# Performance work log

Hardware: AMD Instinct MI355X
Metric: run time of the kernel (lower is better)

The kernel has to match this reference:

```python
import jax, jax.numpy as jnp
import numpy as np

B, N, F_IN, H, E = 8, 10000, 128, 128, 160000


def setup_inputs() -> dict:
    key = jax.random.key(0)
    ks = jax.random.split(key, 6)
    x = jax.random.normal(ks[0], (B, N, F_IN), dtype=jnp.float32)
    edge_index = jax.random.randint(ks[1], (2, E), 0, N, dtype=jnp.int64)
    # GCNConv params (glorot-ish scale), LayerNorm affine params
    W1 = jax.random.normal(ks[2], (F_IN, H), dtype=jnp.float32) / np.sqrt(F_IN)
    b1 = jnp.zeros((H,), dtype=jnp.float32)
    W2 = jax.random.normal(ks[3], (H, H), dtype=jnp.float32) / np.sqrt(H)
    b2 = jnp.zeros((H,), dtype=jnp.float32)
    ln_w = jnp.ones((H,), dtype=jnp.float32)
    ln_b = jnp.zeros((H,), dtype=jnp.float32)
    return {"x": x, "edge_index": edge_index, "W1": W1, "b1": b1,
            "W2": W2, "b2": b2, "ln_w": ln_w, "ln_b": ln_b}


def reference(x, edge_index, W1, b1, W2, b2, ln_w, ln_b):
    # x: [B, N, F]; edge_index: [2, E] shared across batch (tiled per graph
    # in the original via node offsets -> equivalent to vmapping over batch).
    n = x.shape[1]
    loops = jnp.arange(n, dtype=edge_index.dtype)
    src = jnp.concatenate([edge_index[0], loops])  # add self-loops (GCNConv default)
    dst = jnp.concatenate([edge_index[1], loops])
    # symmetric degree normalization: deg over targets with self-loops
    deg = jax.ops.segment_sum(jnp.ones(dst.shape[0], dtype=x.dtype), dst, num_segments=n)
    dinv = jnp.where(deg > 0, jax.lax.rsqrt(deg), 0.0)
    w_e = dinv[src] * dinv[dst]  # [E+N] per-edge norm

    def gcn_agg(h):  # h: [B, N, H] -> gather, scale, scatter-add
        msg = h[:, src, :] * w_e[None, :, None]  # [B, E+N, H]
        return jax.vmap(lambda m: jax.ops.segment_sum(m, dst, num_segments=n))(msg)

    h1 = jax.nn.relu(gcn_agg(x @ W1) + b1)
    h2 = gcn_agg(h1 @ W2) + b2
    # LayerNorm over last dim (eps=1e-5, torch default)
    mu = jnp.mean(h2, axis=-1, keepdims=True)
    var = jnp.mean(jnp.square(h2 - mu), axis=-1, keepdims=True)
    out = (h2 - mu) * jax.lax.rsqrt(var + 1e-5) * ln_w + ln_b
    return out  # [B, N, H]
```

## Files before the change

kernel.cpp:

```cpp
#include <hip/hip_runtime.h>
#include <hip/hip_bf16.h>

#define NNODES 10000
#define NB 8
#define NF 128
#define NE 160000

typedef __attribute__((ext_vector_type(8))) short  short8;
typedef __attribute__((ext_vector_type(8))) unsigned short ushort8;
typedef __attribute__((ext_vector_type(4))) float  f32x4;

__device__ __forceinline__ unsigned short f2b(float f) {
    union { float f; unsigned u; } v; v.f = f;
    unsigned r = v.u + 0x7FFF + ((v.u >> 16) & 1);
    return (unsigned short)(r >> 16);
}
__device__ __forceinline__ unsigned int f2b2(float a, float b) {
    union { __hip_bfloat162 h; unsigned int u; } v;
    v.h = __float22bfloat162_rn(make_float2(a, b));
    return v.u;
}
__device__ __forceinline__ float b2f_lo(unsigned u) {
    union { unsigned u; float f; } v; v.u = u << 16; return v.f;
}
__device__ __forceinline__ float b2f_hi(unsigned u) {
    union { unsigned u; float f; } v; v.u = u & 0xffff0000u; return v.f;
}


__global__ void k_zero(int* __restrict__ cnt, int* __restrict__ fill) {
    int i = blockIdx.x * blockDim.x + threadIdx.x;
    if (i < NNODES) cnt[i] = 0;
    else if (i < 2 * NNODES) fill[i - NNODES] = 0;
}

__global__ void k_count(const int* __restrict__ ei, int* __restrict__ cnt) {
    int e = blockIdx.x * blockDim.x + threadIdx.x;
    if (e < NE) atomicAdd(&cnt[ei[NE + e]], 1);
}

__global__ void k_scan(const int* __restrict__ cnt, int* __restrict__ row_ptr,
                       float* __restrict__ dinv) {
    __shared__ int part[1024];
    int t = threadIdx.x;
    const int CH = (NNODES + 1023) / 1024;
    int lo = t * CH, hi = min(lo + CH, NNODES);
    int s = 0;
    for (int i = lo; i < hi; i++) {
        int c = cnt[i];
        dinv[i] = rsqrtf((float)(c + 1));
        s += c;
    }
    part[t] = s;
    __syncthreads();
    for (int off = 1; off < 1024; off <<= 1) {
        int v = (t >= off) ? part[t - off] : 0;
        __syncthreads();
        part[t] += v;
        __syncthreads();
    }
    int base = part[t] - s;
    for (int i = lo; i < hi; i++) { row_ptr[i] = base; base += cnt[i]; }
    if (t == 1023) row_ptr[NNODES] = part[1023];
}

__global__ void k_scatter(const int* __restrict__ ei, const int* __restrict__ row_ptr,
                          int* __restrict__ fill, const float* __restrict__ dinv,
                          unsigned int* __restrict__ edge) {
    int e = blockIdx.x * blockDim.x + threadIdx.x;
    if (e >= NE) return;
    int s = ei[e];
    int d = ei[NE + e];
    int pos = row_ptr[d] + atomicAdd(&fill[d], 1);
    edge[pos] = (unsigned)s | ((unsigned)f2b(dinv[s] * dinv[d]) << 16);
}

__global__ void k_wt2(const float* __restrict__ W1, unsigned short* __restrict__ Wt1,
                      const float* __restrict__ W2, unsigned short* __restrict__ Wt2) {
    int bid = blockIdx.x;
    const float* W = (bid < 64) ? W1 : W2;
    unsigned short* Wt = (bid < 64) ? Wt1 : Wt2;
    int id = (bid & 63) * 256 + threadIdx.x;
    int n = id >> 7, k = id & 127;
    Wt[(size_t)n * 128 + k] = f2b(W[(size_t)k * 128 + n]);
}

template <bool ABF16>
__global__ __launch_bounds__(256) void k_mm_mfma(const void* __restrict__ Ap,
                                                 const unsigned short* __restrict__ Wt,
                                                 unsigned short* __restrict__ Cn) {
    __shared__ unsigned short wlds[128 * 136];
    const int t = threadIdx.x;
    {
        const int r = t >> 1, h = t & 1;
        const ushort8* src = (const ushort8*)(Wt + r * 128 + h * 64);
        #pragma unroll
        for (int i = 0; i < 8; i++)
            *(ushort8*)(wlds + r * 136 + h * 64 + i * 8) = src[i];
    }
    __syncthreads();

    const int wid = t >> 6, lane = t & 63;
    const int quad = lane >> 4, l16 = lane & 15;
    const int m0 = blockIdx.x * 128 + (wid & 1) * 64;
    const int nb = (wid >> 1) * 64;
    const int kq = quad * 8;

    f32x4 acc[4][4] = {};

    #pragma unroll
    for (int ks = 0; ks < 128; ks += 32) {
        short8 bf[4];
        #pragma unroll
        for (int mi = 0; mi < 4; mi++) {
            const size_t row = (size_t)(m0 + mi * 16 + l16);
            if constexpr (ABF16) {
                bf[mi] = *(const short8*)((const unsigned short*)Ap + row * 128 + ks + kq);
            } else {
                const float* p = (const float*)Ap + row * 128 + ks + kq;
                float4 u0 = *(const float4*)p;
                float4 u1 = *(const float4*)(p + 4);
                union { uint4 u4; short8 s8; } cv;
                cv.u4.x = f2b2(u0.x, u0.y); cv.u4.y = f2b2(u0.z, u0.w);
                cv.u4.z = f2b2(u1.x, u1.y); cv.u4.w = f2b2(u1.z, u1.w);
                bf[mi] = cv.s8;
            }
        }
        short8 af[4];
        #pragma unroll
        for (int ni = 0; ni < 4; ni++)
            af[ni] = *(const short8*)(wlds + (nb + ni * 16 + l16) * 136 + ks + kq);
        #pragma unroll
        for (int mi = 0; mi < 4; mi++)
            #pragma unroll
            for (int ni = 0; ni < 4; ni++)
                acc[mi][ni] = __builtin_amdgcn_mfma_f32_16x16x32_bf16(
                    af[ni], bf[mi], acc[mi][ni], 0, 0, 0);
    }

    __syncthreads();
    {
        const int rbase = (wid & 1) * 64;
        #pragma unroll
        for (int mi = 0; mi < 4; mi++) {
            int rr = rbase + mi * 16 + l16;
            #pragma unroll
            for (int ni = 0; ni < 4; ni++) {
                uint2 p;
                p.x = f2b2(acc[mi][ni][0], acc[mi][ni][1]);
                p.y = f2b2(acc[mi][ni][2], acc[mi][ni][3]);
                *(uint2*)(wlds + rr * 136 + nb + ni * 16 + quad * 4) = p;
            }
        }
    }
    __syncthreads();
    {
        const int r = t >> 1, h = t & 1;
        size_t gm = (size_t)blockIdx.x * 128 + r;
        unsigned short* dst = Cn + gm * 128 + h * 64;
        const unsigned short* srow = wlds + r * 136 + h * 64;
        #pragma unroll
        for (int i = 0; i < 8; i++)
            *(ushort8*)(dst + i * 8) = *(const ushort8*)(srow + i * 8);
    }
}


__global__ __launch_bounds__(256) void k_agg_relu(const unsigned int* __restrict__ hNu,
                                                  const float* __restrict__ bias,
                                                  const int* __restrict__ row_ptr,
                                                  const unsigned int* __restrict__ edge,
                                                  const float* __restrict__ dinv,
                                                  unsigned int* __restrict__ h1u) {
    const int t = threadIdx.x;
    const int b = blockIdx.x & 7;
    const int g = blockIdx.x >> 3;
    const int wid = __builtin_amdgcn_readfirstlane(t >> 6);
    const int lane = t & 63;
    const int n = g * 4 + wid;

    const unsigned int* base = hNu + (size_t)b * NNODES * 64 + lane;
    float di = dinv[n];
    float wself = di * di;
    unsigned int u = base[(size_t)n * 64];
    float a0 = b2f_lo(u) * wself;
    float a1 = b2f_hi(u) * wself;

    int e = row_ptr[n], e1 = row_ptr[n + 1];
    for (; e + 8 <= e1; e += 8) {
        unsigned int E[8];
        #pragma unroll
        for (int j = 0; j < 8; j++) E[j] = edge[e + j];
        unsigned int U[8];
        #pragma unroll
        for (int j = 0; j < 8; j++) U[j] = base[(size_t)(E[j] & 0xffffu) * 64];
        #pragma unroll
        for (int j = 0; j < 8; j++) {
            float w = b2f_hi(E[j]);
            a0 = fmaf(b2f_lo(U[j]), w, a0);
            a1 = fmaf(b2f_hi(U[j]), w, a1);
        }
    }
    for (; e + 4 <= e1; e += 4) {
        unsigned int E[4];
        #pragma unroll
        for (int j = 0; j < 4; j++) E[j] = edge[e + j];
        unsigned int U[4];
        #pragma unroll
        for (int j = 0; j < 4; j++) U[j] = base[(size_t)(E[j] & 0xffffu) * 64];
        #pragma unroll
        for (int j = 0; j < 4; j++) {
            float w = b2f_hi(E[j]);
            a0 = fmaf(b2f_lo(U[j]), w, a0);
            a1 = fmaf(b2f_hi(U[j]), w, a1);
        }
    }
    for (; e < e1; ++e) {
        unsigned int E = edge[e];
        float w = b2f_hi(E);
        unsigned int uu = base[(size_t)(E & 0xffffu) * 64];
        a0 = fmaf(b2f_lo(uu), w, a0);
        a1 = fmaf(b2f_hi(uu), w, a1);
    }
    a0 = fmaxf(a0 + bias[lane * 2], 0.f);
    a1 = fmaxf(a1 + bias[lane * 2 + 1], 0.f);
    __builtin_nontemporal_store(f2b2(a0, a1), &h1u[((size_t)b * NNODES + n) * 64 + lane]);
}

__global__ __launch_bounds__(256) void k_agg_ln(const unsigned int* __restrict__ hNu,
                                                const float* __restrict__ bias,
                                                const int* __restrict__ row_ptr,
                                                const unsigned int* __restrict__ edge,
                                                const float* __restrict__ dinv,
                                                const float* __restrict__ ln_w,
                                                const float* __restrict__ ln_b,
                                                float* __restrict__ out) {
    const int t = threadIdx.x;
    const int b = blockIdx.x & 7;
    const int g = blockIdx.x >> 3;
    const int wid = __builtin_amdgcn_readfirstlane(t >> 6);
    const int lane = t & 63;
    const int n = g * 4 + wid;

    const unsigned int* base = hNu + (size_t)b * NNODES * 64 + lane;
    float di = dinv[n];
    float wself = di * di;
    unsigned int u = base[(size_t)n * 64];
    float a0 = b2f_lo(u) * wself;
    float a1 = b2f_hi(u) * wself;

    int e = row_ptr[n], e1 = row_ptr[n + 1];
    for (; e + 8 <= e1; e += 8) {
        unsigned int E[8];
        #pragma unroll
        for (int j = 0; j < 8; j++) E[j] = edge[e + j];
        unsigned int U[8];
        #pragma unroll
        for (int j = 0; j < 8; j++) U[j] = base[(size_t)(E[j] & 0xffffu) * 64];
        #pragma unroll
        for (int j = 0; j < 8; j++) {
            float w = b2f_hi(E[j]);
            a0 = fmaf(b2f_lo(U[j]), w, a0);
            a1 = fmaf(b2f_hi(U[j]), w, a1);
        }
    }
    for (; e + 4 <= e1; e += 4) {
        unsigned int E[4];
        #pragma unroll
        for (int j = 0; j < 4; j++) E[j] = edge[e + j];
        unsigned int U[4];
        #pragma unroll
        for (int j = 0; j < 4; j++) U[j] = base[(size_t)(E[j] & 0xffffu) * 64];
        #pragma unroll
        for (int j = 0; j < 4; j++) {
            float w = b2f_hi(E[j]);
            a0 = fmaf(b2f_lo(U[j]), w, a0);
            a1 = fmaf(b2f_hi(U[j]), w, a1);
        }
    }
    for (; e < e1; ++e) {
        unsigned int E = edge[e];
        float w = b2f_hi(E);
        unsigned int uu = base[(size_t)(E & 0xffffu) * 64];
        a0 = fmaf(b2f_lo(uu), w, a0);
        a1 = fmaf(b2f_hi(uu), w, a1);
    }
    a0 += bias[lane * 2];
    a1 += bias[lane * 2 + 1];

    float s1 = a0 + a1;
    float s2 = a0 * a0 + a1 * a1;
    #pragma unroll
    for (int m = 1; m < 64; m <<= 1) {
        s1 += __shfl_xor(s1, m);
        s2 += __shfl_xor(s2, m);
    }
    float mu = s1 * (1.f / NF);
    float var = s2 * (1.f / NF) - mu * mu;
    float rs = rsqrtf(var + 1e-5f);

    float o0 = (a0 - mu) * rs * ln_w[lane * 2] + ln_b[lane * 2];
    float o1 = (a1 - mu) * rs * ln_w[lane * 2 + 1] + ln_b[lane * 2 + 1];
    float* dst = out + ((size_t)b * NNODES + n) * 128 + lane * 2;
    __builtin_nontemporal_store(o0, dst);
    __builtin_nontemporal_store(o1, dst + 1);
}


extern "C" void kernel_launch(void* const* d_in, const int* in_sizes, int n_in,
                              void* d_out, int out_size, void* d_ws, size_t ws_size,
                              hipStream_t stream) {
    const float* x    = (const float*)d_in[0];
    const int*   ei   = (const int*)d_in[1];
    const float* W1   = (const float*)d_in[2];
    const float* b1   = (const float*)d_in[3];
    const float* W2   = (const float*)d_in[4];
    const float* b2   = (const float*)d_in[5];
    const float* ln_w = (const float*)d_in[6];
    const float* ln_b = (const float*)d_in[7];
    float* out = (float*)d_out;

    char* ws = (char*)d_ws;
    int*            cnt     = (int*)(ws + 0);
    int*            fill    = (int*)(ws + 40192);
    int*            row_ptr = (int*)(ws + 80384);
    float*          dinv    = (float*)(ws + 120832);
    unsigned int*   edge    = (unsigned int*)(ws + 161024);
    unsigned short* hA16    = (unsigned short*)(ws + 1441024);
    unsigned short* h1b     = (unsigned short*)(ws + 21921024);
    unsigned short* Wt1     = (unsigned short*)cnt;
    unsigned short* Wt2     = (unsigned short*)fill;

    k_zero   <<<(2 * NNODES + 255) / 256, 256, 0, stream>>>(cnt, fill);
    k_count  <<<(NE + 255) / 256, 256, 0, stream>>>(ei, cnt);
    k_scan   <<<1, 1024, 0, stream>>>(cnt, row_ptr, dinv);
    k_scatter<<<(NE + 255) / 256, 256, 0, stream>>>(ei, row_ptr, fill, dinv, edge);
    k_wt2    <<<128, 256, 0, stream>>>(W1, Wt1, W2, Wt2);

    k_mm_mfma<false><<<(NB * NNODES) / 128, 256, 0, stream>>>(x, Wt1, hA16);
    k_agg_relu<<<(NNODES / 4) * NB, 256, 0, stream>>>((const unsigned int*)hA16, b1,
                                                      row_ptr, edge, dinv,
                                                      (unsigned int*)h1b);

    k_mm_mfma<true><<<(NB * NNODES) / 128, 256, 0, stream>>>(h1b, Wt2, hA16);
    k_agg_ln<<<(NNODES / 4) * NB, 256, 0, stream>>>((const unsigned int*)hA16, b2,
                                                    row_ptr, edge, dinv,
                                                    ln_w, ln_b, out);
}
```

Measured before the change: 230.0 us.

## Use wave-shuffle scan, read weights directly from global, memset instead of zero kernel

Replaces the LDS Hillis-Steele scan in k_scan with a two-level wave shuffle scan and keeps counts in registers, removing about twenty block barriers. In k_mm_mfma the weight-tile staging into LDS and its barrier are dropped, so weight fragments are read straight from global or L2 memory. The zero kernel is replaced by hipMemsetAsync. The trade-off is that weight reads in the matmul are now repeated global loads instead of LDS hits, which could slow the GEMM if L2 does not absorb them.

Result: no change. 233.4 us (+1.5%).

```diff
diff --git a/kernel.cpp b/kernel.cpp
--- a/kernel.cpp
+++ b/kernel.cpp
@@ -28,40 +28,49 @@
 }
 
 
-__global__ void k_zero(int* __restrict__ cnt, int* __restrict__ fill) {
-    int i = blockIdx.x * blockDim.x + threadIdx.x;
-    if (i < NNODES) cnt[i] = 0;
-    else if (i < 2 * NNODES) fill[i - NNODES] = 0;
-}
-
 __global__ void k_count(const int* __restrict__ ei, int* __restrict__ cnt) {
     int e = blockIdx.x * blockDim.x + threadIdx.x;
     if (e < NE) atomicAdd(&cnt[ei[NE + e]], 1);
 }
 
-__global__ void k_scan(const int* __restrict__ cnt, int* __restrict__ row_ptr,
-                       float* __restrict__ dinv) {
-    __shared__ int part[1024];
-    int t = threadIdx.x;
-    const int CH = (NNODES + 1023) / 1024;
-    int lo = t * CH, hi = min(lo + CH, NNODES);
+__global__ __launch_bounds__(1024) void k_scan(const int* __restrict__ cnt,
+                                               int* __restrict__ row_ptr,
+                                               float* __restrict__ dinv) {
+    __shared__ int wsum[16];
+    const int t = threadIdx.x;
+    const int lane = t & 63, wv = t >> 6;
+    const int CH = 10;
+    int lo = t * CH;
+    int hi = min(lo + CH, NNODES);
+    int c10[CH];
     int s = 0;
     for (int i = lo; i < hi; i++) {
         int c = cnt[i];
+        c10[i - lo] = c;
         dinv[i] = rsqrtf((float)(c + 1));
         s += c;
     }
-    part[t] = s;
+    int v = s;
+    #pragma unroll
+    for (int m = 1; m < 64; m <<= 1) {
+        int o = __shfl_up(v, m);
+        if (lane >= m) v += o;
+    }
+    if (lane == 63) wsum[wv] = v;
     __syncthreads();
-    for (int off = 1; off < 1024; off <<= 1) {
-        int v = (t >= off) ? part[t - off] : 0;
-        __syncthreads();
-        part[t] += v;
-        __syncthreads();
-    }
-    int base = part[t] - s;
-    for (int i = lo; i < hi; i++) { row_ptr[i] = base; base += cnt[i]; }
-    if (t == 1023) row_ptr[NNODES] = part[1023];
+    if (t < 16) {
+        int w = wsum[t];
+        #pragma unroll
+        for (int m = 1; m < 16; m <<= 1) {
+            int o = __shfl_up(w, m);
+            if (t >= m) w += o;
+        }
+        wsum[t] = w;
+    }
+    __syncthreads();
+    int base = v - s + (wv ? wsum[wv - 1] : 0);
+    for (int i = lo; i < hi; i++) { row_ptr[i] = base; base += c10[i - lo]; }
+    if (t == 1023) row_ptr[NNODES] = wsum[15];
 }
 
 __global__ void k_scatter(const int* __restrict__ ei, const int* __restrict__ row_ptr,
@@ -89,17 +98,8 @@
 __global__ __launch_bounds__(256) void k_mm_mfma(const void* __restrict__ Ap,
                                                  const unsigned short* __restrict__ Wt,
                                                  unsigned short* __restrict__ Cn) {
-    __shared__ unsigned short wlds[128 * 136];
+    __shared__ unsigned short clds[128 * 136];
     const int t = threadIdx.x;
-    {
-        const int r = t >> 1, h = t & 1;
-        const ushort8* src = (const ushort8*)(Wt + r * 128 + h * 64);
-        #pragma unroll
-        for (int i = 0; i < 8; i++)
-            *(ushort8*)(wlds + r * 136 + h * 64 + i * 8) = src[i];
-    }
-    __syncthreads();
-
     const int wid = t >> 6, lane = t & 63;
     const int quad = lane >> 4, l16 = lane & 15;
     const int m0 = blockIdx.x * 128 + (wid & 1) * 64;
@@ -110,6 +110,10 @@
 
     #pragma unroll
     for (int ks = 0; ks < 128; ks += 32) {
+        short8 af[4];
+        #pragma unroll
+        for (int ni = 0; ni < 4; ni++)
+            af[ni] = *(const short8*)(Wt + (size_t)(nb + ni * 16 + l16) * 128 + ks + kq);
         short8 bf[4];
         #pragma unroll
         for (int mi = 0; mi < 4; mi++) {
@@ -126,10 +130,6 @@
                 bf[mi] = cv.s8;
             }
         }
-        short8 af[4];
-        #pragma unroll
-        for (int ni = 0; ni < 4; ni++)
-            af[ni] = *(const short8*)(wlds + (nb + ni * 16 + l16) * 136 + ks + kq);
         #pragma unroll
         for (int mi = 0; mi < 4; mi++)
             #pragma unroll
@@ -138,7 +138,6 @@
                     af[ni], bf[mi], acc[mi][ni], 0, 0, 0);
     }
 
-    __syncthreads();
     {
         const int rbase = (wid & 1) * 64;
         #pragma unroll
@@ -149,7 +148,7 @@
                 uint2 p;
                 p.x = f2b2(acc[mi][ni][0], acc[mi][ni][1]);
                 p.y = f2b2(acc[mi][ni][2], acc[mi][ni][3]);
-                *(uint2*)(wlds + rr * 136 + nb + ni * 16 + quad * 4) = p;
+                *(uint2*)(clds + rr * 136 + nb + ni * 16 + quad * 4) = p;
             }
         }
     }
@@ -158,7 +157,7 @@
         const int r = t >> 1, h = t & 1;
         size_t gm = (size_t)blockIdx.x * 128 + r;
         unsigned short* dst = Cn + gm * 128 + h * 64;
-        const unsigned short* srow = wlds + r * 136 + h * 64;
+        const unsigned short* srow = clds + r * 136 + h * 64;
         #pragma unroll
         for (int i = 0; i < 8; i++)
             *(ushort8*)(dst + i * 8) = *(const ushort8*)(srow + i * 8);
@@ -331,7 +330,7 @@
     unsigned short* Wt1     = (unsigned short*)cnt;
     unsigned short* Wt2     = (unsigned short*)fill;
 
-    k_zero   <<<(2 * NNODES + 255) / 256, 256, 0, stream>>>(cnt, fill);
+    hipMemsetAsync(ws, 0, 80384, stream);
     k_count  <<<(NE + 255) / 256, 256, 0, stream>>>(ei, cnt);
     k_scan   <<<1, 1024, 0, stream>>>(cnt, row_ptr, dinv);
     k_scatter<<<(NE + 255) / 256, 256, 0, stream>>>(ei, row_ptr, fill, dinv, edge);
```
